# Optimization experiments

Measured on AMD Instinct MI355X. Metric: run time of the kernel, lower is better.

Reference implementation:

```python
import jax, jax.numpy as jnp
import numpy as np
from jax import lax

H_HEADS = 8      # attention heads
C_HID = 32       # per-head channels
NEG_SLOPE = 0.2  # PyG GATConv default leaky_relu slope


def _gat(x, src, dst, W, a_src, a_dst, b, num_nodes):
    # x: (N, Din); src/dst: (E',) with self-loops already appended
    h = (x @ W).reshape(num_nodes, H_HEADS, C_HID)          # (N, H, C)
    e = jax.nn.leaky_relu((h * a_src).sum(-1)[src] + (h * a_dst).sum(-1)[dst], NEG_SLOPE)  # (E', H)
    emax = jax.ops.segment_max(e, dst, num_segments=num_nodes)
    ex = jnp.exp(e - emax[dst])
    denom = jax.ops.segment_sum(ex, dst, num_segments=num_nodes)
    alpha = ex / (denom[dst] + 1e-16)                        # segment softmax over incoming edges
    out = jax.ops.segment_sum(h[src] * alpha[:, :, None], dst, num_segments=num_nodes)
    return out.reshape(num_nodes, H_HEADS * C_HID) + b


def _lstm_dir(seq, Wih, Whh, bih, bhh):
    # seq: (K, D); single-direction LSTM, returns final hidden state (Hs,)
    Hs = Whh.shape[1]
    def step(carry, x):
        h, c = carry
        g = x @ Wih.T + h @ Whh.T + bih + bhh                # (4*Hs,)
        i, f, gg, o = jnp.split(g, 4)
        c = jax.nn.sigmoid(f) * c + jax.nn.sigmoid(i) * jnp.tanh(gg)
        h = jax.nn.sigmoid(o) * jnp.tanh(c)
        return (h, c), None
    (h, _), _ = lax.scan(step, (jnp.zeros(Hs, seq.dtype), jnp.zeros(Hs, seq.dtype)), seq)
    return h


def setup_inputs():
    key = jax.random.key(0)
    ks = jax.random.split(key, 20)
    K, N, E = 8, 10000, 160000
    D1, D2, LH = 1, H_HEADS * C_HID, 256   # D2 = 256
    s = 0.1
    inp = {}
    inp['xs'] = jax.random.normal(ks[0], (K, N, D1), jnp.float32)
    inp['edge_index'] = jax.random.randint(ks[1], (K, 2, E), 0, N, jnp.int32)
    inp['W1'] = jax.random.normal(ks[2], (D1, D2), jnp.float32) * s
    inp['a_src1'] = jax.random.normal(ks[3], (H_HEADS, C_HID), jnp.float32) * s
    inp['a_dst1'] = jax.random.normal(ks[4], (H_HEADS, C_HID), jnp.float32) * s
    inp['b1'] = jnp.zeros((D2,), jnp.float32)
    inp['W2'] = jax.random.normal(ks[5], (D2, D2), jnp.float32) * s
    inp['a_src2'] = jax.random.normal(ks[6], (H_HEADS, C_HID), jnp.float32) * s
    inp['a_dst2'] = jax.random.normal(ks[7], (H_HEADS, C_HID), jnp.float32) * s
    inp['b2'] = jnp.zeros((D2,), jnp.float32)
    inp['Wih_f'] = jax.random.normal(ks[8], (4 * LH, D2), jnp.float32) * s
    inp['Whh_f'] = jax.random.normal(ks[9], (4 * LH, LH), jnp.float32) * s
    inp['bih_f'] = jnp.zeros((4 * LH,), jnp.float32)
    inp['bhh_f'] = jnp.zeros((4 * LH,), jnp.float32)
    inp['Wih_b'] = jax.random.normal(ks[10], (4 * LH, D2), jnp.float32) * s
    inp['Whh_b'] = jax.random.normal(ks[11], (4 * LH, LH), jnp.float32) * s
    inp['bih_b'] = jnp.zeros((4 * LH,), jnp.float32)
    inp['bhh_b'] = jnp.zeros((4 * LH,), jnp.float32)
    return inp


def reference(xs, edge_index, W1, a_src1, a_dst1, b1, W2, a_src2, a_dst2, b2,
              Wih_f, Whh_f, bih_f, bhh_f, Wih_b, Whh_b, bih_b, bhh_b):
    N = xs.shape[1]
    loops = jnp.arange(N, dtype=edge_index.dtype)  # self-loops (PyG default)
    def snap(carry, inp):
        x, ei = inp
        src = jnp.concatenate([ei[0], loops])
        dst = jnp.concatenate([ei[1], loops])
        h = jax.nn.relu(_gat(x, src, dst, W1, a_src1, a_dst1, b1, N))
        h = jax.nn.relu(_gat(h, src, dst, W2, a_src2, a_dst2, b2, N))
        return carry, h.mean(0)   # global mean pool -> (256,)
    _, embs = lax.scan(snap, 0, (xs, edge_index))   # (K, 256)
    h_fwd = _lstm_dir(embs, Wih_f, Whh_f, bih_f, bhh_f)
    h_bwd = _lstm_dir(embs[::-1], Wih_b, Whh_b, bih_b, bhh_b)
    return jnp.concatenate([h_fwd, h_bwd])[None, :]  # (1, 512)
```

## Files before the change

kernel.cpp:

```cpp
#include <hip/hip_runtime.h>
#include <math.h>

#define H_HEADS 8
#define C_HID 32
#define D2 256
#define NEG_SLOPE 0.2f
#define KSTEPS 8

__device__ __forceinline__ float lrelu(float x) { return x < 0.f ? NEG_SLOPE * x : x; }
__device__ __forceinline__ float sigmoidf(float x) { return 1.f / (1.f + expf(-x)); }


__global__ void zero_all_kernel(int* counts, int* fill, double* embp, int KN, int NEMBP,
                                const float* __restrict__ W1, const float* __restrict__ a_src1,
                                const float* __restrict__ a_dst1, float* Pvec, int D1) {
    int tid = blockIdx.x * blockDim.x + threadIdx.x;
    if (tid < KN) { counts[tid] = 0; fill[tid] = 0; }
    if (tid < NEMBP) embp[tid] = 0.0;
    if (blockIdx.x == 0 && threadIdx.x < 16 && D1 == 1) {
        int h = threadIdx.x & 7;
        const float* a = (threadIdx.x >= 8) ? a_dst1 : a_src1;
        float s = 0.f;
        for (int c = 0; c < 32; ++c) s += W1[h * 32 + c] * a[h * 32 + c];
        Pvec[threadIdx.x] = s;
    }
}


__global__ void count_all_kernel(const int* __restrict__ ei, int E, int N, int K,
                                 int* __restrict__ counts) {
    int bid = blockIdx.x;
    int k = bid % K;
    int jb = bid / K;
    int j = jb * blockDim.x + threadIdx.x;
    if (j >= E + N) return;
    int d = (j < E) ? ei[(size_t)k * 2 * E + E + j] : (j - E);
    atomicAdd(&counts[(size_t)k * N + d], 1);
}

__global__ __launch_bounds__(1024) void scan_all_kernel(const int* __restrict__ counts,
                                                        int* __restrict__ row_ptr, int N) {
    int k = blockIdx.x;
    const int* cnt = counts + (size_t)k * N;
    int* rp = row_ptr + (size_t)k * (N + 1);
    __shared__ int part[1024];
    int t = threadIdx.x;
    int ipt = (N + 1023) >> 10;
    int begin = t * ipt;
    int end = begin + ipt; if (end > N) end = N;
    if (begin > N) begin = N;
    int s = 0;
    for (int i = begin; i < end; ++i) s += cnt[i];
    part[t] = s;
    __syncthreads();
    for (int d = 1; d < 1024; d <<= 1) {
        int v = 0;
        if (t >= d) v = part[t - d];
        __syncthreads();
        if (t >= d) part[t] += v;
        __syncthreads();
    }
    int run = (t == 0) ? 0 : part[t - 1];
    for (int i = begin; i < end; ++i) { rp[i] = run; run += cnt[i]; }
    if (t == 1023) rp[N] = part[1023];
}

__global__ void scatter_all_kernel(const int* __restrict__ ei, int E, int N, int K,
                                   const int* __restrict__ row_ptr, int* __restrict__ fill,
                                   int* __restrict__ ein) {
    int bid = blockIdx.x;
    int k = bid % K;
    int jb = bid / K;
    int j = jb * blockDim.x + threadIdx.x;
    if (j >= E + N) return;
    int s, d;
    if (j < E) { s = ei[(size_t)k * 2 * E + j]; d = ei[(size_t)k * 2 * E + E + j]; }
    else { s = j - E; d = s; }
    int pos = row_ptr[(size_t)k * (N + 1) + d] + atomicAdd(&fill[(size_t)k * N + d], 1);
    ein[(size_t)k * (E + N) + pos] = s;
}


__global__ __launch_bounds__(256) void agg1s_all_kernel(const float* __restrict__ xs,
                                                        const float* __restrict__ P,
                                                        const int* __restrict__ row_ptr,
                                                        const int* __restrict__ ein,
                                                        float* __restrict__ Sbuf,
                                                        int N, int E2, int k0, int BKcur) {
    int bid = blockIdx.x;
    int kb = bid % BKcur;
    int nb = bid / BKcur;
    int k = k0 + kb;
    const float* x = xs + (size_t)k * N;
    const int* rp = row_ptr + (size_t)k * (N + 1);
    const int* ek = ein + (size_t)k * E2;

    int n = nb * 4 + (threadIdx.x >> 6);
    if (n >= N) return;
    int lane = threadIdx.x & 63;
    int e0 = rp[n], e1 = rp[n + 1];
    int h8 = lane & 7;
    float Ps = P[h8], Pd = P[8 + h8];
    float base = x[n] * Pd;

    float mx = -INFINITY;
    for (int i = e0 + (lane >> 3); i < e1; i += 8) {
        float xv = x[ek[i]];
        mx = fmaxf(mx, lrelu(xv * Ps + base));
    }
    mx = fmaxf(mx, __shfl_xor(mx, 8));
    mx = fmaxf(mx, __shfl_xor(mx, 16));
    mx = fmaxf(mx, __shfl_xor(mx, 32));

    float num = 0.f, den = 0.f;
    for (int i = e0 + (lane >> 3); i < e1; i += 8) {
        float xv = x[ek[i]];
        float w = expf(lrelu(xv * Ps + base) - mx);
        num += w * xv;
        den += w;
    }
    num += __shfl_xor(num, 8);  den += __shfl_xor(den, 8);
    num += __shfl_xor(num, 16); den += __shfl_xor(den, 16);
    num += __shfl_xor(num, 32); den += __shfl_xor(den, 32);
    float S = num / (den + 1e-16f);

    if (lane < 8) Sbuf[((size_t)kb * N + n) * 8 + lane] = S;
}


__global__ void h1_kernel(const float* __restrict__ x, const float* __restrict__ W,
                          float* __restrict__ h, int N, int D1) {
    int tid = blockIdx.x * blockDim.x + threadIdx.x;
    if (tid >= N * 256) return;
    int n = tid >> 8, j = tid & 255;
    float acc = 0.f;
    for (int d = 0; d < D1; ++d) acc += x[n * D1 + d] * W[d * 256 + j];
    h[tid] = acc;
}

__global__ __launch_bounds__(256) void s_all_kernel(const float* __restrict__ bufA,
                                                    const float* __restrict__ a_src,
                                                    const float* __restrict__ a_dst,
                                                    float* __restrict__ s_src,
                                                    float* __restrict__ s_dst, int N) {
    int kb = blockIdx.y;
    int j = blockIdx.x * 256 + threadIdx.x;
    if (j >= N * 8) return;
    int n = j >> 3, hh = j & 7;
    const float* hp = bufA + (size_t)kb * N * 256 + (size_t)n * 256 + hh * 32;
    const float* as = a_src + hh * 32;
    const float* ad = a_dst + hh * 32;
    float ss = 0.f, sd = 0.f;
#pragma unroll
    for (int c = 0; c < 32; ++c) { float v = hp[c]; ss += v * as[c]; sd += v * ad[c]; }
    s_src[(size_t)kb * N * 8 + j] = ss;
    s_dst[(size_t)kb * N * 8 + j] = sd;
}

__global__ __launch_bounds__(256) void agg2_out_kernel(const float* __restrict__ h,
                                                       const float* __restrict__ s_src,
                                                       const float* __restrict__ s_dst,
                                                       const int* __restrict__ row_ptr,
                                                       const int* __restrict__ ein,
                                                       const float* __restrict__ bias,
                                                       float* __restrict__ out,
                                                       int N, int E2, int k0) {
    int k = k0;
    const int* rp = row_ptr + (size_t)k * (N + 1);
    const int* ek = ein + (size_t)k * E2;
    int n = blockIdx.x * 4 + (threadIdx.x >> 6);
    if (n >= N) return;
    int lane = threadIdx.x & 63;
    int e0 = rp[n], e1 = rp[n + 1];
    int h8 = lane & 7;
    float sd8 = s_dst[n * 8 + h8];

    float mx = -INFINITY;
    for (int i = e0 + (lane >> 3); i < e1; i += 8) {
        int s = ek[i];
        mx = fmaxf(mx, lrelu(s_src[s * 8 + h8] + sd8));
    }
    mx = fmaxf(mx, __shfl_xor(mx, 8));
    mx = fmaxf(mx, __shfl_xor(mx, 16));
    mx = fmaxf(mx, __shfl_xor(mx, 32));

    int hd = lane >> 3;
    float m = __shfl(mx, hd);
    float sdh = __shfl(sd8, hd);

    float den = 0.f;
    float4 acc = make_float4(0.f, 0.f, 0.f, 0.f);
    for (int i = e0; i < e1; ++i) {
        int s = ek[i];
        const float4 hv = *(const float4*)(h + (size_t)s * 256 + lane * 4);
        float w = expf(lrelu(s_src[s * 8 + hd] + sdh) - m);
        den += w;
        acc.x += w * hv.x; acc.y += w * hv.y; acc.z += w * hv.z; acc.w += w * hv.w;
    }
    float dE = den + 1e-16f;
    const float4 bv = *(const float4*)(bias + lane * 4);
    float4 o;
    o.x = fmaxf(acc.x / dE + bv.x, 0.f);
    o.y = fmaxf(acc.y / dE + bv.y, 0.f);
    o.z = fmaxf(acc.z / dE + bv.z, 0.f);
    o.w = fmaxf(acc.w / dE + bv.w, 0.f);
    *(float4*)(out + (size_t)n * 256 + lane * 4) = o;
}


__global__ __launch_bounds__(256) void agg2pool_kernel(const float* __restrict__ bufA,
                                                       const float* __restrict__ s_src,
                                                       const float* __restrict__ s_dst,
                                                       const int* __restrict__ row_ptr,
                                                       const int* __restrict__ ein,
                                                       const float* __restrict__ bias,
                                                       double* __restrict__ embp,
                                                       int N, int E2, int k0, int BKcur) {
    int bid = blockIdx.x;
    int kb = bid % BKcur;
    int nb = bid / BKcur;
    int k = k0 + kb;
    int w = threadIdx.x >> 6;
    int lane = threadIdx.x & 63;
    int n = nb * 4 + w;
    bool active = (n < N);
    const float* h = bufA + (size_t)kb * N * 256;
    const float* ssrc = s_src + (size_t)kb * N * 8;
    const float* sdst = s_dst + (size_t)kb * N * 8;
    const int* rp = row_ptr + (size_t)k * (N + 1);
    const int* ek = ein + (size_t)k * E2;

    float4 o = make_float4(0.f, 0.f, 0.f, 0.f);
    if (active) {
        int e0 = rp[n], e1 = rp[n + 1];
        int h8 = lane & 7;
        int es = lane >> 3;
        int hd = lane >> 3;
        float sd8 = sdst[n * 8 + h8];

        float mx = -INFINITY;
        for (int i = e0 + es; i < e1; i += 8) {
            int s = ek[i];
            mx = fmaxf(mx, lrelu(ssrc[s * 8 + h8] + sd8));
        }
        mx = fmaxf(mx, __shfl_xor(mx, 8));
        mx = fmaxf(mx, __shfl_xor(mx, 16));
        mx = fmaxf(mx, __shfl_xor(mx, 32));

        float den = 0.f;
        float4 acc = make_float4(0.f, 0.f, 0.f, 0.f);
        int hd4 = hd;

        for (int c0 = e0; c0 < e1; c0 += 8) {
            int eI = c0 + es;
            bool valid = (eI < e1);
            int sA = ek[valid ? eI : e0];
            float wv = expf(lrelu(ssrc[sA * 8 + h8] + sd8) - mx);
            if (!valid) wv = 0.f;

            int jmax = e1 - c0; if (jmax > 8) jmax = 8;
#pragma unroll 8
            for (int j = 0; j < 8; ++j) {
                if (j >= jmax) break;
                int srcLane = (j << 3) + hd4;
                float wj = __shfl(wv, srcLane);
                int sj = __shfl(sA, srcLane);
                const float4 hv = *(const float4*)(h + (size_t)sj * 256 + lane * 4);
                den += wj;
                acc.x += wj * hv.x;
                acc.y += wj * hv.y;
                acc.z += wj * hv.z;
                acc.w += wj * hv.w;
            }
        }
        float dE = den + 1e-16f;
        const float4 bv = *(const float4*)(bias + lane * 4);
        o.x = fmaxf(acc.x / dE + bv.x, 0.f);
        o.y = fmaxf(acc.y / dE + bv.y, 0.f);
        o.z = fmaxf(acc.z / dE + bv.z, 0.f);
        o.w = fmaxf(acc.w / dE + bv.w, 0.f);
    }

    __shared__ double pe[4][256];
    pe[w][lane * 4 + 0] = (double)o.x;
    pe[w][lane * 4 + 1] = (double)o.y;
    pe[w][lane * 4 + 2] = (double)o.z;
    pe[w][lane * 4 + 3] = (double)o.w;
    __syncthreads();
    int tid = threadIdx.x;
    double s = pe[0][tid] + pe[1][tid] + pe[2][tid] + pe[3][tid];
    atomicAdd(&embp[((size_t)k * 32 + (nb & 31)) * 256 + tid], s);
}


__global__ __launch_bounds__(256) void gemm_fused_kernel(const float* __restrict__ S,
                                                         const float* __restrict__ W1,
                                                         const float* __restrict__ bias1,
                                                         const float* __restrict__ B,
                                                         float* __restrict__ C, int M) {
    __shared__ float Ast[16][132];
    __shared__ float Bs[16][132];
    __shared__ float w1s[256], b1s[256];
    __shared__ float Ss[128 * 8];
    int tid = threadIdx.x;
    int bm = blockIdx.x, bn = blockIdx.y;

    w1s[tid] = W1[tid];
    b1s[tid] = bias1[tid];
    {
        int base = bm * 128 * 8 + tid * 4;
        float4 sv = make_float4(0.f, 0.f, 0.f, 0.f);
        if (bm * 128 + (tid * 4) / 8 < M) {
            sv = *(const float4*)(S + base);
        }
        *(float4*)&Ss[tid * 4] = sv;
    }

    int arow = tid >> 1;
    int kgrp = (tid & 1) * 8;
    bool rowvalid = (bm * 128 + arow < M);

    int brow = tid >> 4;
    int bcol = (tid & 15) * 8;
    const float* Bbase = B + bn * 128;

    int w = tid >> 6, lane = tid & 63;
    int qr = (w >> 1) * 64, qc = (w & 1) * 64;
    int ty = lane >> 3, tx = lane & 7;
    int r0 = qr + ty * 8, c0 = qc + tx * 8;
    float acc[8][8] = {};

    __syncthreads();

    for (int kt = 0; kt < 256; kt += 16) {
        float sh = Ss[arow * 8 + (kt >> 5)];
#pragma unroll
        for (int j = 0; j < 8; ++j) {
            int kk = kgrp + j;
            float a = fmaxf(fmaf(sh, w1s[kt + kk], b1s[kt + kk]), 0.f);
            Ast[kk][arow] = rowvalid ? a : 0.f;
        }
        const float* bg = Bbase + (size_t)(kt + brow) * 256 + bcol;
        *(float4*)&Bs[brow][bcol] = *(const float4*)bg;
        *(float4*)&Bs[brow][bcol + 4] = *(const float4*)(bg + 4);
        __syncthreads();
#pragma unroll
        for (int kk = 0; kk < 16; ++kk) {
            float4 a0 = *(const float4*)&Ast[kk][r0];
            float4 a1 = *(const float4*)&Ast[kk][r0 + 4];
            float4 b0 = *(const float4*)&Bs[kk][c0];
            float4 b1v = *(const float4*)&Bs[kk][c0 + 4];
            float ar[8] = {a0.x, a0.y, a0.z, a0.w, a1.x, a1.y, a1.z, a1.w};
            float br[8] = {b0.x, b0.y, b0.z, b0.w, b1v.x, b1v.y, b1v.z, b1v.w};
#pragma unroll
            for (int i2 = 0; i2 < 8; ++i2)
#pragma unroll
                for (int j2 = 0; j2 < 8; ++j2) acc[i2][j2] += ar[i2] * br[j2];
        }
        __syncthreads();
    }
#pragma unroll
    for (int i2 = 0; i2 < 8; ++i2) {
        int gm = bm * 128 + r0 + i2;
        if (gm < M) {
            *(float4*)(C + (size_t)gm * 256 + bn * 128 + c0) =
                make_float4(acc[i2][0], acc[i2][1], acc[i2][2], acc[i2][3]);
            *(float4*)(C + (size_t)gm * 256 + bn * 128 + c0 + 4) =
                make_float4(acc[i2][4], acc[i2][5], acc[i2][6], acc[i2][7]);
        }
    }
}


__global__ __launch_bounds__(256) void gemm_kernel(const float* __restrict__ A,
                                                   const float* __restrict__ B,
                                                   float* __restrict__ C, int M) {
    __shared__ float Ast[8][132];
    __shared__ float Bs[8][128];
    int tid = threadIdx.x;
    int bm = blockIdx.x, bn = blockIdx.y;
    int ty = tid >> 4, tx = tid & 15;
    int r0 = ty * 8, c0 = tx * 8;
    float acc[8][8] = {};
    int arow = tid >> 1, acol = (tid & 1) * 4;
    int brow = tid >> 5, bcol = (tid & 31) * 4;
    const float* Bbase = B + bn * 128;

    for (int kt = 0; kt < 256; kt += 8) {
        int gr = bm * 128 + arow;
        float4 av = (gr < M) ? *(const float4*)(A + (size_t)gr * 256 + kt + acol)
                             : make_float4(0.f, 0.f, 0.f, 0.f);
        Ast[acol + 0][arow] = av.x;
        Ast[acol + 1][arow] = av.y;
        Ast[acol + 2][arow] = av.z;
        Ast[acol + 3][arow] = av.w;
        *(float4*)&Bs[brow][bcol] = *(const float4*)(Bbase + (size_t)(kt + brow) * 256 + bcol);
        __syncthreads();
#pragma unroll
        for (int kk = 0; kk < 8; ++kk) {
            float4 a0 = *(const float4*)&Ast[kk][r0];
            float4 a1 = *(const float4*)&Ast[kk][r0 + 4];
            float4 b0 = *(const float4*)&Bs[kk][c0];
            float4 b1 = *(const float4*)&Bs[kk][c0 + 4];
            float ar[8] = {a0.x, a0.y, a0.z, a0.w, a1.x, a1.y, a1.z, a1.w};
            float br[8] = {b0.x, b0.y, b0.z, b0.w, b1.x, b1.y, b1.z, b1.w};
#pragma unroll
            for (int i2 = 0; i2 < 8; ++i2)
#pragma unroll
                for (int j2 = 0; j2 < 8; ++j2) acc[i2][j2] += ar[i2] * br[j2];
        }
        __syncthreads();
    }
#pragma unroll
    for (int i2 = 0; i2 < 8; ++i2) {
        int gm = bm * 128 + r0 + i2;
        if (gm < M) {
            *(float4*)(C + (size_t)gm * 256 + bn * 128 + c0) =
                make_float4(acc[i2][0], acc[i2][1], acc[i2][2], acc[i2][3]);
            *(float4*)(C + (size_t)gm * 256 + bn * 128 + c0 + 4) =
                make_float4(acc[i2][4], acc[i2][5], acc[i2][6], acc[i2][7]);
        }
    }
}


__global__ void merge_kernel(const double* __restrict__ embp, float* __restrict__ emb,
                             int* __restrict__ flags) {
    int k = blockIdx.x, c = threadIdx.x;
    double s = 0.0;
#pragma unroll
    for (int p = 0; p < 32; ++p) s += embp[((size_t)k * 32 + p) * 256 + c];
    emb[k * 256 + c] = (float)s;
    if (blockIdx.x == 0 && threadIdx.x < 2 * (KSTEPS + 1)) flags[threadIdx.x] = 0;
}


__global__ __launch_bounds__(256) void lstm_rec_kernel(
    const float* __restrict__ emb, float invN,
    const float* __restrict__ Wih_f, const float* __restrict__ Whh_f,
    const float* __restrict__ bih_f, const float* __restrict__ bhh_f,
    const float* __restrict__ Wih_b, const float* __restrict__ Whh_b,
    const float* __restrict__ bih_b, const float* __restrict__ bhh_b,
    float* __restrict__ hbuf, int* __restrict__ flags, float* __restrict__ out) {
    int dir = blockIdx.x >> 4;
    int seg = blockIdx.x & 15;
    const float* Wih = dir ? Wih_b : Wih_f;
    const float* Whh = dir ? Whh_b : Whh_f;
    const float* bih = dir ? bih_b : bih_f;
    const float* bhh = dir ? bhh_b : bhh_f;

    __shared__ float wh[64 * 256];
    __shared__ float wi[64 * 256];
    __shared__ float xs_s[KSTEPS * 256];
    __shared__ float gx[KSTEPS][64];
    __shared__ float garr[64];
    __shared__ float hprev_s[256];
    int tid = threadIdx.x;

    for (int v = tid; v < 64 * 64; v += 256) {
        int lrow = v >> 6;
        int c4 = (v & 63) * 4;
        int grow = ((lrow >> 4) << 8) + seg * 16 + (lrow & 15);
        *(float4*)&wh[lrow * 256 + c4] = *(const float4*)(Whh + (size_t)grow * 256 + c4);
        *(float4*)&wi[lrow * 256 + c4] = *(const float4*)(Wih + (size_t)grow * 256 + c4);
    }
    for (int idx = tid; idx < KSTEPS * 256; idx += 256) xs_s[idx] = emb[idx] * invN;
    __syncthreads();

    for (int d = tid; d < KSTEPS * 64; d += 256) {
        int st = d >> 6, lr = d & 63;
        const float* wr = &wi[lr << 8];
        const float* xr = &xs_s[st << 8];
        int r = (tid & 63) << 2;
        float acc = 0.f;
#pragma unroll 8
        for (int kk = 0; kk < 256; kk += 4) {
            int k2 = (kk + r) & 255;
            acc += wr[k2] * xr[k2] + wr[k2 + 1] * xr[k2 + 1] +
                   wr[k2 + 2] * xr[k2 + 2] + wr[k2 + 3] * xr[k2 + 3];
        }
        int grow = ((lr >> 4) << 8) + seg * 16 + (lr & 15);
        gx[st][lr] = acc + bih[grow] + bhh[grow];
    }

    int* flag = flags + dir * (KSTEPS + 1);
    float* hb = hbuf + dir * (KSTEPS + 1) * 256;

    if (tid < 16)
        __hip_atomic_store(&hb[seg * 16 + tid], 0.f, __ATOMIC_RELAXED, __HIP_MEMORY_SCOPE_AGENT);
    __syncthreads();
    if (tid == 0)
        __hip_atomic_fetch_add(&flag[0], 1, __ATOMIC_RELEASE, __HIP_MEMORY_SCOPE_AGENT);

    float c_reg = 0.f;

    for (int step = 0; step < KSTEPS; ++step) {
        if (tid == 0) {
            while (__hip_atomic_load(&flag[step], __ATOMIC_RELAXED, __HIP_MEMORY_SCOPE_AGENT) < 16) {
                __builtin_amdgcn_s_sleep(1);
            }
            (void)__hip_atomic_load(&flag[step], __ATOMIC_ACQUIRE, __HIP_MEMORY_SCOPE_AGENT);
        }
        __syncthreads();
        hprev_s[tid] = __hip_atomic_load(&hb[step * 256 + tid], __ATOMIC_RELAXED,
                                         __HIP_MEMORY_SCOPE_AGENT);
        __syncthreads();

        int d = tid >> 2, p = tid & 3;
        const float* wr = &wh[(d << 8) + (p << 6)];
        const float* hr = &hprev_s[p << 6];
        int rot = tid & 63;
        float acc = 0.f;
#pragma unroll 8
        for (int k = 0; k < 64; ++k) {
            int k2 = (k + rot) & 63;
            acc += wr[k2] * hr[k2];
        }
        acc += __shfl_xor(acc, 1);
        acc += __shfl_xor(acc, 2);
        if (p == 0) garr[d] = acc;
        __syncthreads();

        if (tid < 16) {
            float ig = sigmoidf(garr[tid] + gx[step][tid]);
            float fg = sigmoidf(garr[16 + tid] + gx[step][16 + tid]);
            float gg = tanhf(garr[32 + tid] + gx[step][32 + tid]);
            float og = sigmoidf(garr[48 + tid] + gx[step][48 + tid]);
            float cn = fg * c_reg + ig * gg;
            c_reg = cn;
            float hn = og * tanhf(cn);
            __hip_atomic_store(&hb[(step + 1) * 256 + seg * 16 + tid], hn, __ATOMIC_RELAXED,
                               __HIP_MEMORY_SCOPE_AGENT);
        }
        __syncthreads();
        if (tid == 0)
            __hip_atomic_fetch_add(&flag[step + 1], 1, __ATOMIC_RELEASE, __HIP_MEMORY_SCOPE_AGENT);
    }

    if (tid < 16)
        out[dir * 256 + seg * 16 + tid] =
            __hip_atomic_load(&hb[KSTEPS * 256 + seg * 16 + tid], __ATOMIC_RELAXED,
                              __HIP_MEMORY_SCOPE_AGENT);
}


extern "C" void kernel_launch(void* const* d_in, const int* in_sizes, int n_in,
                              void* d_out, int out_size, void* d_ws, size_t ws_size,
                              hipStream_t stream) {
    const float* xs = (const float*)d_in[0];
    const int* edge_index = (const int*)d_in[1];
    const float* W1 = (const float*)d_in[2];
    const float* a_src1 = (const float*)d_in[3];
    const float* a_dst1 = (const float*)d_in[4];
    const float* b1 = (const float*)d_in[5];
    const float* W2 = (const float*)d_in[6];
    const float* a_src2 = (const float*)d_in[7];
    const float* a_dst2 = (const float*)d_in[8];
    const float* b2 = (const float*)d_in[9];
    const float* Wih_f = (const float*)d_in[10];
    const float* Whh_f = (const float*)d_in[11];
    const float* bih_f = (const float*)d_in[12];
    const float* bhh_f = (const float*)d_in[13];
    const float* Wih_b = (const float*)d_in[14];
    const float* Whh_b = (const float*)d_in[15];
    const float* bih_b = (const float*)d_in[16];
    const float* bhh_b = (const float*)d_in[17];

    const int K = KSTEPS;
    int D1 = in_sizes[2] / D2;
    int N = in_sizes[0] / (K * D1);
    int E = in_sizes[1] / (2 * K);
    int E2 = E + N;

    auto al = [](size_t x) { return (x + 255) & ~(size_t)255; };
    size_t fixed_sz = al((size_t)K * N * 4)
                    + al((size_t)K * (N + 1) * 4)
                    + al((size_t)K * N * 4)
                    + al((size_t)K * E2 * 4)
                    + al((size_t)K * 32 * 256 * 8)
                    + al((size_t)K * 256 * 4)
                    + al((size_t)2 * (K + 1) * 256 * 4)
                    + al((size_t)2 * (K + 1) * 4)
                    + al(16 * 4);
    int BK = 8;
    while (BK > 1) {
        size_t need = fixed_sz + 3 * al((size_t)BK * N * 8 * 4) + 2 * al((size_t)BK * N * 256 * 4);
        if (need <= ws_size) break;
        BK >>= 1;
    }

    char* w = (char*)d_ws;
    auto alloc = [&](size_t bytes) { char* p = w; w += (bytes + 255) & ~(size_t)255; return p; };
    int* counts = (int*)alloc((size_t)K * N * 4);
    int* row_ptr = (int*)alloc((size_t)K * (N + 1) * 4);
    int* fill = (int*)alloc((size_t)K * N * 4);
    int* ein = (int*)alloc((size_t)K * E2 * 4);
    double* embp = (double*)alloc((size_t)K * 32 * 256 * 8);
    float* emb = (float*)alloc((size_t)K * 256 * 4);
    float* hbuf = (float*)alloc((size_t)2 * (K + 1) * 256 * 4);
    int* flags = (int*)alloc((size_t)2 * (K + 1) * 4);
    float* Pvec = (float*)alloc(16 * 4);
    float* Sbuf = (float*)alloc((size_t)BK * N * 8 * 4);
    float* s_src = (float*)alloc((size_t)BK * N * 8 * 4);
    float* s_dst = (float*)alloc((size_t)BK * N * 8 * 4);
    float* bufA = (float*)alloc((size_t)BK * N * 256 * 4);
    float* bufB = (float*)alloc((size_t)BK * N * 256 * 4);

    int KN = K * N;
    int NEMBP = K * 32 * 256;
    int zblk = ((KN > NEMBP ? KN : NEMBP) + 255) / 256;
    zero_all_kernel<<<zblk, 256, 0, stream>>>(counts, fill, embp, KN, NEMBP,
                                              W1, a_src1, a_dst1, Pvec, D1);
    int eblk = (E2 + 255) / 256;
    count_all_kernel<<<eblk * K, 256, 0, stream>>>(edge_index, E, N, K, counts);
    scan_all_kernel<<<K, 1024, 0, stream>>>(counts, row_ptr, N);
    scatter_all_kernel<<<eblk * K, 256, 0, stream>>>(edge_index, E, N, K, row_ptr, fill, ein);

    int nblk4 = (N + 3) / 4;
    int sblk = (N * 8 + 255) / 256;
    for (int k0 = 0; k0 < K; k0 += BK) {
        int BKcur = (K - k0 < BK) ? (K - k0) : BK;
        if (D1 == 1) {
            agg1s_all_kernel<<<nblk4 * BKcur, 256, 0, stream>>>(
                xs, Pvec, row_ptr, ein, Sbuf, N, E2, k0, BKcur);
            int M = BKcur * N;
            gemm_fused_kernel<<<dim3((M + 127) / 128, 2), 256, 0, stream>>>(
                Sbuf, W1, b1, W2, bufA, M);
            s_all_kernel<<<dim3(sblk, BKcur), 256, 0, stream>>>(bufA, a_src2, a_dst2,
                                                                s_src, s_dst, N);
            agg2pool_kernel<<<nblk4 * BKcur, 256, 0, stream>>>(
                bufA, s_src, s_dst, row_ptr, ein, b2, embp, N, E2, k0, BKcur);
        } else {
            for (int kk = 0; kk < BKcur; ++kk) {
                int k = k0 + kk;
                const float* xk = xs + (size_t)k * N * D1;
                h1_kernel<<<(N * 256 + 255) / 256, 256, 0, stream>>>(xk, W1, bufA, N, D1);
                s_all_kernel<<<dim3(sblk, 1), 256, 0, stream>>>(bufA, a_src1, a_dst1,
                                                                s_src, s_dst, N);
                agg2_out_kernel<<<nblk4, 256, 0, stream>>>(bufA, s_src, s_dst, row_ptr, ein,
                                                           b1, bufB, N, E2, k);
                gemm_kernel<<<dim3((N + 127) / 128, 2), 256, 0, stream>>>(bufB, W2, bufA, N);
                s_all_kernel<<<dim3(sblk, 1), 256, 0, stream>>>(bufA, a_src2, a_dst2,
                                                                s_src, s_dst, N);
                agg2pool_kernel<<<nblk4, 256, 0, stream>>>(
                    bufA, s_src, s_dst, row_ptr, ein, b2, embp, N, E2, k, 1);
            }
        }
    }

    merge_kernel<<<K, 256, 0, stream>>>(embp, emb, flags);
    lstm_rec_kernel<<<32, 256, 0, stream>>>(emb, 1.f / (float)N,
                                            Wih_f, Whh_f, bih_f, bhh_f,
                                            Wih_b, Whh_b, bih_b, bhh_b,
                                            hbuf, flags, (float*)d_out);
}
```

Before: 582.8 us.

## Bucket CSR edges by source range within each destination row

Extends the CSR build so that each destination's incoming edges are grouped into 4 buckets by source node range, using a composite key of destination and source bucket. Aggregation kernels read row bounds at bucket granularity, and the layer-2 pooled aggregation loops over buckets. The aim is to improve locality of the gathered 1 KB feature rows, so waves working on nearby nodes touch similar source regions at the same time and hit in cache more often. In exchange the count, fill and row_ptr arrays are four times larger, the scan has more work, and the per-bucket loop leaves more partial 8-edge chunks.

```diff
diff --git a/kernel.cpp b/kernel.cpp
--- a/kernel.cpp
+++ b/kernel.cpp
@@ -6,16 +6,17 @@
 #define D2 256
 #define NEG_SLOPE 0.2f
 #define KSTEPS 8
+#define NBUCK 4
 
 __device__ __forceinline__ float lrelu(float x) { return x < 0.f ? NEG_SLOPE * x : x; }
 __device__ __forceinline__ float sigmoidf(float x) { return 1.f / (1.f + expf(-x)); }
 
 
-__global__ void zero_all_kernel(int* counts, int* fill, double* embp, int KN, int NEMBP,
+__global__ void zero_all_kernel(int* counts, int* fill, double* embp, int KNB, int NEMBP,
                                 const float* __restrict__ W1, const float* __restrict__ a_src1,
                                 const float* __restrict__ a_dst1, float* Pvec, int D1) {
     int tid = blockIdx.x * blockDim.x + threadIdx.x;
-    if (tid < KN) { counts[tid] = 0; fill[tid] = 0; }
+    if (tid < KNB) { counts[tid] = 0; fill[tid] = 0; }
     if (tid < NEMBP) embp[tid] = 0.0;
     if (blockIdx.x == 0 && threadIdx.x < 16 && D1 == 1) {
         int h = threadIdx.x & 7;
@@ -27,28 +28,31 @@
 }
 
 
-__global__ void count_all_kernel(const int* __restrict__ ei, int E, int N, int K,
+__global__ void count_all_kernel(const int* __restrict__ ei, int E, int N, int K, int bsz,
                                  int* __restrict__ counts) {
     int bid = blockIdx.x;
     int k = bid % K;
     int jb = bid / K;
     int j = jb * blockDim.x + threadIdx.x;
     if (j >= E + N) return;
-    int d = (j < E) ? ei[(size_t)k * 2 * E + E + j] : (j - E);
-    atomicAdd(&counts[(size_t)k * N + d], 1);
+    int s, d;
+    if (j < E) { s = ei[(size_t)k * 2 * E + j]; d = ei[(size_t)k * 2 * E + E + j]; }
+    else { s = j - E; d = s; }
+    int key = d * NBUCK + s / bsz;
+    atomicAdd(&counts[(size_t)k * N * NBUCK + key], 1);
 }
 
 __global__ __launch_bounds__(1024) void scan_all_kernel(const int* __restrict__ counts,
-                                                        int* __restrict__ row_ptr, int N) {
+                                                        int* __restrict__ row_ptr, int Nk) {
     int k = blockIdx.x;
-    const int* cnt = counts + (size_t)k * N;
-    int* rp = row_ptr + (size_t)k * (N + 1);
+    const int* cnt = counts + (size_t)k * Nk;
+    int* rp = row_ptr + (size_t)k * (Nk + 1);
     __shared__ int part[1024];
     int t = threadIdx.x;
-    int ipt = (N + 1023) >> 10;
+    int ipt = (Nk + 1023) >> 10;
     int begin = t * ipt;
-    int end = begin + ipt; if (end > N) end = N;
-    if (begin > N) begin = N;
+    int end = begin + ipt; if (end > Nk) end = Nk;
+    if (begin > Nk) begin = Nk;
     int s = 0;
     for (int i = begin; i < end; ++i) s += cnt[i];
     part[t] = s;
@@ -62,10 +66,10 @@
     }
     int run = (t == 0) ? 0 : part[t - 1];
     for (int i = begin; i < end; ++i) { rp[i] = run; run += cnt[i]; }
-    if (t == 1023) rp[N] = part[1023];
-}
-
-__global__ void scatter_all_kernel(const int* __restrict__ ei, int E, int N, int K,
+    if (t == 1023) rp[Nk] = part[1023];
+}
+
+__global__ void scatter_all_kernel(const int* __restrict__ ei, int E, int N, int K, int bsz,
                                    const int* __restrict__ row_ptr, int* __restrict__ fill,
                                    int* __restrict__ ein) {
     int bid = blockIdx.x;
@@ -76,7 +80,9 @@
     int s, d;
     if (j < E) { s = ei[(size_t)k * 2 * E + j]; d = ei[(size_t)k * 2 * E + E + j]; }
     else { s = j - E; d = s; }
-    int pos = row_ptr[(size_t)k * (N + 1) + d] + atomicAdd(&fill[(size_t)k * N + d], 1);
+    int key = d * NBUCK + s / bsz;
+    int pos = row_ptr[(size_t)k * (N * NBUCK + 1) + key] +
+              atomicAdd(&fill[(size_t)k * N * NBUCK + key], 1);
     ein[(size_t)k * (E + N) + pos] = s;
 }
 
@@ -92,13 +98,13 @@
     int nb = bid / BKcur;
     int k = k0 + kb;
     const float* x = xs + (size_t)k * N;
-    const int* rp = row_ptr + (size_t)k * (N + 1);
+    const int* rp = row_ptr + (size_t)k * (N * NBUCK + 1);
     const int* ek = ein + (size_t)k * E2;
 
     int n = nb * 4 + (threadIdx.x >> 6);
     if (n >= N) return;
     int lane = threadIdx.x & 63;
-    int e0 = rp[n], e1 = rp[n + 1];
+    int e0 = rp[n * NBUCK], e1 = rp[(n + 1) * NBUCK];
     int h8 = lane & 7;
     float Ps = P[h8], Pd = P[8 + h8];
     float base = x[n] * Pd;
@@ -166,12 +172,12 @@
                                                        float* __restrict__ out,
                                                        int N, int E2, int k0) {
     int k = k0;
-    const int* rp = row_ptr + (size_t)k * (N + 1);
+    const int* rp = row_ptr + (size_t)k * (N * NBUCK + 1);
     const int* ek = ein + (size_t)k * E2;
     int n = blockIdx.x * 4 + (threadIdx.x >> 6);
     if (n >= N) return;
     int lane = threadIdx.x & 63;
-    int e0 = rp[n], e1 = rp[n + 1];
+    int e0 = rp[n * NBUCK], e1 = rp[(n + 1) * NBUCK];
     int h8 = lane & 7;
     float sd8 = s_dst[n * 8 + h8];
 
@@ -227,12 +233,12 @@
     const float* h = bufA + (size_t)kb * N * 256;
     const float* ssrc = s_src + (size_t)kb * N * 8;
     const float* sdst = s_dst + (size_t)kb * N * 8;
-    const int* rp = row_ptr + (size_t)k * (N + 1);
+    const int* rp = row_ptr + (size_t)k * (N * NBUCK + 1);
     const int* ek = ein + (size_t)k * E2;
 
     float4 o = make_float4(0.f, 0.f, 0.f, 0.f);
     if (active) {
-        int e0 = rp[n], e1 = rp[n + 1];
+        int e0 = rp[n * NBUCK], e1 = rp[(n + 1) * NBUCK];
         int h8 = lane & 7;
         int es = lane >> 3;
         int hd = lane >> 3;
@@ -249,28 +255,30 @@
 
         float den = 0.f;
         float4 acc = make_float4(0.f, 0.f, 0.f, 0.f);
-        int hd4 = hd;
-
-        for (int c0 = e0; c0 < e1; c0 += 8) {
-            int eI = c0 + es;
-            bool valid = (eI < e1);
-            int sA = ek[valid ? eI : e0];
-            float wv = expf(lrelu(ssrc[sA * 8 + h8] + sd8) - mx);
-            if (!valid) wv = 0.f;
-
-            int jmax = e1 - c0; if (jmax > 8) jmax = 8;
+
+        for (int b = 0; b < NBUCK; ++b) {
+            int be0 = rp[n * NBUCK + b], be1 = rp[n * NBUCK + b + 1];
+            for (int c0 = be0; c0 < be1; c0 += 8) {
+                int eI = c0 + es;
+                bool valid = (eI < be1);
+                int sA = ek[valid ? eI : be0];
+                float wv = expf(lrelu(ssrc[sA * 8 + h8] + sd8) - mx);
+                if (!valid) wv = 0.f;
+
+                int jmax = be1 - c0; if (jmax > 8) jmax = 8;
 #pragma unroll 8
-            for (int j = 0; j < 8; ++j) {
-                if (j >= jmax) break;
-                int srcLane = (j << 3) + hd4;
-                float wj = __shfl(wv, srcLane);
-                int sj = __shfl(sA, srcLane);
-                const float4 hv = *(const float4*)(h + (size_t)sj * 256 + lane * 4);
-                den += wj;
-                acc.x += wj * hv.x;
-                acc.y += wj * hv.y;
-                acc.z += wj * hv.z;
-                acc.w += wj * hv.w;
+                for (int j = 0; j < 8; ++j) {
+                    if (j >= jmax) break;
+                    int srcLane = (j << 3) + hd;
+                    float wj = __shfl(wv, srcLane);
+                    int sj = __shfl(sA, srcLane);
+                    const float4 hv = *(const float4*)(h + (size_t)sj * 256 + lane * 4);
+                    den += wj;
+                    acc.x += wj * hv.x;
+                    acc.y += wj * hv.y;
+                    acc.z += wj * hv.z;
+                    acc.w += wj * hv.w;
+                }
             }
         }
         float dE = den + 1e-16f;
@@ -571,11 +579,13 @@
     int N = in_sizes[0] / (K * D1);
     int E = in_sizes[1] / (2 * K);
     int E2 = E + N;
+    int Nk = N * NBUCK;
+    int bsz = (N + NBUCK - 1) / NBUCK;
 
     auto al = [](size_t x) { return (x + 255) & ~(size_t)255; };
-    size_t fixed_sz = al((size_t)K * N * 4)
-                    + al((size_t)K * (N + 1) * 4)
-                    + al((size_t)K * N * 4)
+    size_t fixed_sz = al((size_t)K * Nk * 4)
+                    + al((size_t)K * (Nk + 1) * 4)
+                    + al((size_t)K * Nk * 4)
                     + al((size_t)K * E2 * 4)
                     + al((size_t)K * 32 * 256 * 8)
                     + al((size_t)K * 256 * 4)
@@ -591,9 +601,9 @@
 
     char* w = (char*)d_ws;
     auto alloc = [&](size_t bytes) { char* p = w; w += (bytes + 255) & ~(size_t)255; return p; };
-    int* counts = (int*)alloc((size_t)K * N * 4);
-    int* row_ptr = (int*)alloc((size_t)K * (N + 1) * 4);
-    int* fill = (int*)alloc((size_t)K * N * 4);
+    int* counts = (int*)alloc((size_t)K * Nk * 4);
+    int* row_ptr = (int*)alloc((size_t)K * (Nk + 1) * 4);
+    int* fill = (int*)alloc((size_t)K * Nk * 4);
     int* ein = (int*)alloc((size_t)K * E2 * 4);
     double* embp = (double*)alloc((size_t)K * 32 * 256 * 8);
     float* emb = (float*)alloc((size_t)K * 256 * 4);
@@ -606,15 +616,15 @@
     float* bufA = (float*)alloc((size_t)BK * N * 256 * 4);
     float* bufB = (float*)alloc((size_t)BK * N * 256 * 4);
 
-    int KN = K * N;
+    int KNB = K * Nk;
     int NEMBP = K * 32 * 256;
-    int zblk = ((KN > NEMBP ? KN : NEMBP) + 255) / 256;
-    zero_all_kernel<<<zblk, 256, 0, stream>>>(counts, fill, embp, KN, NEMBP,
+    int zblk = ((KNB > NEMBP ? KNB : NEMBP) + 255) / 256;
+    zero_all_kernel<<<zblk, 256, 0, stream>>>(counts, fill, embp, KNB, NEMBP,
                                               W1, a_src1, a_dst1, Pvec, D1);
     int eblk = (E2 + 255) / 256;
-    count_all_kernel<<<eblk * K, 256, 0, stream>>>(edge_index, E, N, K, counts);
-    scan_all_kernel<<<K, 1024, 0, stream>>>(counts, row_ptr, N);
-    scatter_all_kernel<<<eblk * K, 256, 0, stream>>>(edge_index, E, N, K, row_ptr, fill, ein);
+    count_all_kernel<<<eblk * K, 256, 0, stream>>>(edge_index, E, N, K, bsz, counts);
+    scan_all_kernel<<<K, 1024, 0, stream>>>(counts, row_ptr, Nk);
+    scatter_all_kernel<<<eblk * K, 256, 0, stream>>>(edge_index, E, N, K, bsz, row_ptr, fill, ein);
 
     int nblk4 = (N + 3) / 4;
     int sblk = (N * 8 + 255) / 256;
```

Measured after the change: 654.4 us. +12.3%, slower.
